# Optimization experiments

Hardware: AMD Instinct MI355X
Metric: run time of the kernel (lower is better)

The kernel has to match this reference:

```python
import jax, jax.numpy as jnp
import numpy as np

N_LAYERS = 6
EPS = 1e-5


def _s4d_layer(u, log_dt, C_re, C_im, log_A_real, A_imag, D, out_w, out_b):
    # u: (B, H, L). Standard S4D: diagonal SSM kernel -> FFT conv -> D skip -> GELU -> 1x1 conv + GLU.
    B, H, L = u.shape
    dt = jnp.exp(log_dt)                                   # (H,)
    A = -jnp.exp(log_A_real) + 1j * A_imag                 # (H, N2) complex
    dtA = A * dt[:, None]                                  # (H, N2)
    C = (C_re + 1j * C_im) * (jnp.exp(dtA) - 1.0) / A      # (H, N2) ZOH-discretized C
    V = jnp.exp(dtA[:, :, None] * jnp.arange(L))           # (H, N2, L) Vandermonde exp(dtA * l)
    k = 2.0 * jnp.einsum('hn,hnl->hl', C, V).real          # (H, L) SSM convolution kernel
    # circular conv via length-2L FFT (equivalent to causal linear conv, then truncate)
    k_f = jnp.fft.rfft(k, n=2 * L)                         # (H, L+1)
    u_f = jnp.fft.rfft(u, n=2 * L)                         # (B, H, L+1)
    y = jnp.fft.irfft(u_f * k_f, n=2 * L)[..., :L]         # (B, H, L)
    y = y + u * D[:, None]                                 # skip connection
    y = jax.nn.gelu(y, approximate=False)                  # torch nn.GELU (exact erf)
    y = jnp.einsum('bhl,gh->bgl', y, out_w) + out_b[:, None]  # 1x1 Conv1d -> (B, 2H, L)
    a, b = jnp.split(y, 2, axis=1)                         # GLU over channel dim (dim=-2)
    return a * jax.nn.sigmoid(b)


def _batchnorm(x, gamma, beta):
    # BatchNorm1d over (B, H, L): per-channel stats across batch and length (training-mode forward)
    mean = x.mean(axis=(0, 2), keepdims=True)
    var = x.var(axis=(0, 2), keepdims=True)
    return (x - mean) * jax.lax.rsqrt(var + EPS) * gamma[None, :, None] + beta[None, :, None]


def setup_inputs() -> dict:
    B, L, D_IN, H, N2 = 8, 5000, 12, 256, 32
    key = jax.random.key(0)
    ks = jax.random.split(key, 8)
    x = jax.random.normal(ks[0], (B, L, D_IN), jnp.float32)
    pre_w = jax.random.normal(ks[1], (H, D_IN), jnp.float32) / np.float32(np.sqrt(D_IN))
    pre_b = jnp.zeros((H,), jnp.float32)
    # log_dt ~ Uniform(log 0.001, log 0.1) as in S4DKernel init
    log_dt = (jax.random.uniform(ks[2], (N_LAYERS, H), jnp.float32)
              * np.float32(np.log(0.1) - np.log(0.001)) + np.float32(np.log(0.001)))
    C_re = jax.random.normal(ks[3], (N_LAYERS, H, N2), jnp.float32)
    C_im = jax.random.normal(ks[4], (N_LAYERS, H, N2), jnp.float32)
    log_A_real = jnp.full((N_LAYERS, H, N2), np.float32(np.log(0.5)), jnp.float32)
    A_imag = jnp.broadcast_to(np.float32(np.pi) * jnp.arange(N2, dtype=jnp.float32),
                              (N_LAYERS, H, N2)) + jnp.zeros((N_LAYERS, H, N2), jnp.float32)
    D = jax.random.normal(ks[5], (N_LAYERS, H), jnp.float32)
    out_w = jax.random.normal(ks[6], (N_LAYERS, 2 * H, H), jnp.float32) / np.float32(np.sqrt(H))
    out_b = jnp.zeros((N_LAYERS, 2 * H), jnp.float32)
    bn_gamma = jnp.ones((3, H), jnp.float32)
    bn_beta = jnp.zeros((3, H), jnp.float32)
    return {"x": x, "pre_w": pre_w, "pre_b": pre_b, "log_dt": log_dt, "C_re": C_re,
            "C_im": C_im, "log_A_real": log_A_real, "A_imag": A_imag, "D": D,
            "out_w": out_w, "out_b": out_b, "bn_gamma": bn_gamma, "bn_beta": bn_beta}


def reference(x, pre_w, pre_b, log_dt, C_re, C_im, log_A_real, A_imag, D, out_w, out_b, bn_gamma, bn_beta):
    h = x @ pre_w.T + pre_b          # (B, L, H) pre-projection
    h = jnp.swapaxes(h, -1, -2)      # (B, H, L)
    bn_idx = 0
    for i in range(N_LAYERS):
        z = _s4d_layer(h, log_dt[i], C_re[i], C_im[i], log_A_real[i], A_imag[i],
                       D[i], out_w[i], out_b[i])
        h = z + h                     # residual (dropout is identity in eval/reference)
        if i % 2 == 0:                # BatchNorm1d on even layers only
            h = _batchnorm(h, bn_gamma[bn_idx], bn_beta[bn_idx])
            bn_idx += 1
    return jnp.swapaxes(h, -1, -2)   # (B, L, H)
```

## Files before the change

### kernel.cpp

```cpp
#include <hip/hip_runtime.h>
#include <hip/hip_bf16.h>
#include <math.h>

#define NB 8
#define LSEQ 5000
#define DIN 12
#define HCH 256
#define N2C 32
#define NLAY 6
#define G2C 512
#define TTC 64
#define NCH 79
#define LPAD 5120

typedef __attribute__((ext_vector_type(8))) short bf8v;
typedef __attribute__((ext_vector_type(8))) unsigned short us8v;
typedef __attribute__((ext_vector_type(4))) float f32x4;

#define MFMA16(a,b,c) __builtin_amdgcn_mfma_f32_16x16x32_bf16((a),(b),(c),0,0,0)

static __device__ __forceinline__ unsigned short f2bf(float f){
  unsigned int u = __float_as_uint(f);
  u = u + 0x7FFFu + ((u >> 16) & 1u);
  return (unsigned short)(u >> 16);
}
static __device__ __forceinline__ float bf2f(unsigned short s){
  return __uint_as_float(((unsigned int)s) << 16);
}
static __device__ __forceinline__ bf8v pack8(float4 a, float4 b){
  bf8v r;
  r[0]=(short)f2bf(a.x); r[1]=(short)f2bf(a.y); r[2]=(short)f2bf(a.z); r[3]=(short)f2bf(a.w);
  r[4]=(short)f2bf(b.x); r[5]=(short)f2bf(b.y); r[6]=(short)f2bf(b.z); r[7]=(short)f2bf(b.w);
  return r;
}
static __device__ __forceinline__ float gelu_f(float x){
  return 0.5f*x*(1.0f + erff(x*0.70710678118654752f));
}
static __device__ __forceinline__ float sigm(float x){
  return 1.0f/(1.0f + expf(-x));
}


__global__ __launch_bounds__(256) void kp_params(
    const float* __restrict__ log_dt, const float* __restrict__ lAr,
    const float* __restrict__ A_im, const float* __restrict__ C_re,
    const float* __restrict__ C_im,
    float* __restrict__ p_ar, float* __restrict__ p_ai,
    float* __restrict__ p_cer, float* __restrict__ p_cei,
    float* __restrict__ p_wtr, float* __restrict__ p_wti)
{
  int idx = blockIdx.x*256 + threadIdx.x;
  int lh = idx >> 5;
  float dt = expf(log_dt[lh]);
  float Are = -expf(lAr[idx]);
  float Aim = A_im[idx];
  float ar = Are*dt, ai = Aim*dt;
  float er = expf(ar);
  float wr = er*cosf(ai), wi = er*sinf(ai);
  float inv = 1.0f/(Are*Are + Aim*Aim);
  float tr = ((wr-1.0f)*Are + wi*Aim)*inv;
  float ti = (wi*Are - (wr-1.0f)*Aim)*inv;
  p_cer[idx] = C_re[idx]*tr - C_im[idx]*ti;
  p_cei[idx] = C_re[idx]*ti + C_im[idx]*tr;
  p_ar[idx] = ar; p_ai[idx] = ai;
  float eT = expf(ar*64.0f);
  p_wtr[idx] = eT*cosf(ai*64.0f);
  p_wti[idx] = eT*sinf(ai*64.0f);
}

__global__ __launch_bounds__(256) void kp_kk(
    const float* __restrict__ p_ar, const float* __restrict__ p_ai,
    const float* __restrict__ p_cer, const float* __restrict__ p_cei,
    float* __restrict__ kk)
{
  int idx = blockIdx.x*256 + threadIdx.x;
  int d = idx & 63, lh = idx >> 6;
  int base = lh*N2C;
  float fd = (float)d;
  float s = 0.0f;
  for (int n=0; n<N2C; n++){
    float ar = p_ar[base+n], ai = p_ai[base+n];
    float e = expf(ar*fd);
    float pr = e*cosf(ai*fd), pi = e*sinf(ai*fd);
    s += p_cer[base+n]*pr - p_cei[base+n]*pi;
  }
  kk[idx] = 2.0f*s;
}

__global__ __launch_bounds__(256) void kp_A2(
    const float* __restrict__ p_ar, const float* __restrict__ p_ai,
    const float* __restrict__ p_cer, const float* __restrict__ p_cei,
    const float* __restrict__ kk, unsigned short* __restrict__ A2b)
{
  int idx = blockIdx.x*256 + threadIdx.x;
  int kcol = idx & 127;
  int t = (idx >> 7) & 63;
  int lh = idx >> 13;
  float v;
  if (kcol < 64){
    v = (kcol <= t) ? kk[lh*64 + (t - kcol)] : 0.0f;
  } else {
    int q = kcol - 64, n = q >> 1;
    int p = lh*N2C + n;
    float fp = (float)(t+1);
    float e = expf(p_ar[p]*fp);
    float pr = e*cosf(p_ai[p]*fp), pi = e*sinf(p_ai[p]*fp);
    float cer = p_cer[p], cei = p_cei[p];
    v = (q&1) ? -2.0f*(cer*pi + cei*pr) : 2.0f*(cer*pr - cei*pi);
  }
  A2b[idx] = f2bf(v);
}

__global__ __launch_bounds__(256) void kp_Vm(
    const float* __restrict__ p_ar, const float* __restrict__ p_ai,
    unsigned short* __restrict__ Vmb)
{
  int idx = blockIdx.x*256 + threadIdx.x;
  int j = idx & 63;
  int q = (idx >> 6) & 63;
  int lh = idx >> 12;
  int n = q >> 1;
  int p = lh*N2C + n;
  float fp = (float)(63 - j);
  float e = expf(p_ar[p]*fp);
  float pr = e*cosf(p_ai[p]*fp), pi = e*sinf(p_ai[p]*fp);
  Vmb[idx] = f2bf((q&1) ? pi : pr);
}

__global__ __launch_bounds__(256) void kp_Wp(
    const float* __restrict__ out_w, const float* __restrict__ out_b,
    unsigned short* __restrict__ Wpb, float* __restrict__ bp)
{
  int idx = blockIdx.x*256 + threadIdx.x;
  int hcol = idx & 255;
  int g2 = (idx >> 8) & 511;
  int li = idx >> 17;
  int src = (g2 >> 1) + ((g2 & 1) ? HCH : 0);
  Wpb[idx] = f2bf(out_w[((size_t)li*G2C + src)*HCH + hcol]);
  if (hcol == 0) bp[li*G2C + g2] = out_b[li*G2C + src];
}


__global__ __launch_bounds__(256) void k_preproj(
    const float* __restrict__ x, const float* __restrict__ pre_w,
    const float* __restrict__ pre_b, float* __restrict__ hbuf)
{
  int l = blockIdx.x*256 + threadIdx.x;
  int hc = blockIdx.y, b = blockIdx.z;
  if (l >= LSEQ) return;
  const float* xr = x + (size_t)(b*LSEQ + l)*DIN;
  const float* wr = pre_w + hc*DIN;
  float acc = pre_b[hc];
  #pragma unroll
  for (int d=0; d<DIN; d++) acc += xr[d]*wr[d];
  hbuf[(size_t)(b*HCH + hc)*LSEQ + l] = acc;
}


template<int DO_BN>
__global__ __launch_bounds__(320, 4) void k_row(
    const unsigned short* __restrict__ Vm, const unsigned short* __restrict__ A2,
    const float* __restrict__ wtr, const float* __restrict__ wti,
    const float* __restrict__ Dg, float* __restrict__ hbuf,
    const float* __restrict__ scale, const float* __restrict__ shift,
    unsigned short* __restrict__ yg, int layer)
{
  __shared__ float su[5120];
  __shared__ float sE[5120];
  int bh = blockIdx.x;
  int hc = bh & (HCH-1);
  int tid = threadIdx.x, wid = tid>>6, lane = tid&63;
  float* hrow = hbuf + (size_t)bh*LSEQ;
  float bsc = 1.0f, bsh = 0.0f;
  if (DO_BN){ bsc = scale[hc]; bsh = shift[hc]; }
  #pragma unroll
  for (int i=0;i<4;i++){
    int q = tid + i*320;
    float4 v = {0,0,0,0};
    if (q < 1250) v = *(const float4*)(hrow + q*4);
    if (DO_BN){
      v.x=v.x*bsc+bsh; v.y=v.y*bsc+bsh; v.z=v.z*bsc+bsh; v.w=v.w*bsc+bsh;
      if (q < 1250) *(float4*)(hrow + q*4) = v;
    }
    int p = q ^ (((q>>4)&7)<<1);
    *(float4*)(su + p*4) = v;
  }
  __syncthreads();

  int craw = wid*16 + (lane&15);
  int c = craw < NCH ? craw : NCH-1;
  int krow8 = (lane>>4)*8;
  int swz = (c&7)<<1;

  {
    const unsigned short* Vp = Vm + (size_t)(layer*HCH + hc)*TTC*TTC + (size_t)(lane&15)*TTC;
    f32x4 a0={0,0,0,0},a1={0,0,0,0},a2={0,0,0,0},a3={0,0,0,0};
    #pragma unroll
    for (int ks=0; ks<2; ks++){
      int kb = ks*32 + krow8;
      int p0 = (c*16 + (kb>>2)) ^ swz;
      float4 u0 = *(const float4*)(su + p0*4);
      float4 u1 = *(const float4*)(su + p0*4 + 4);
      bf8v bfr = pack8(u0,u1);
      a0 = MFMA16(*(const bf8v*)(Vp + 0*16*TTC + kb), bfr, a0);
      a1 = MFMA16(*(const bf8v*)(Vp + 1*16*TTC + kb), bfr, a1);
      a2 = MFMA16(*(const bf8v*)(Vp + 2*16*TTC + kb), bfr, a2);
      a3 = MFMA16(*(const bf8v*)(Vp + 3*16*TTC + kb), bfr, a3);
    }
    if (craw < NCH){
      int j0 = craw*16 + (lane>>4);
      int sw2 = (craw&7)<<1;
      *(f32x4*)(sE + (size_t)((j0+ 0)^sw2)*4) = a0;
      *(f32x4*)(sE + (size_t)((j0+ 4)^sw2)*4) = a1;
      *(f32x4*)(sE + (size_t)((j0+ 8)^sw2)*4) = a2;
      *(f32x4*)(sE + (size_t)((j0+12)^sw2)*4) = a3;
    }
  }
  __syncthreads();

  if (tid < 256){
    int n = tid >> 3, g = tid & 7;
    float wr = wtr[(layer*HCH+hc)*N2C + n];
    float wi = wti[(layer*HCH+hc)*N2C + n];
    int c0 = g*10;
    int cnt = NCH - c0; if (cnt > 10) cnt = 10;
    float er[10], ei[10];
    #pragma unroll
    for (int k=0;k<10;k++){
      if (k < cnt){
        int cc = c0 + k;
        int p = ((cc*16 + (n>>1)) ^ ((cc&7)<<1))*4 + (n&1)*2;
        er[k] = sE[p]; ei[k] = sE[p+1];
      } else { er[k]=0.0f; ei[k]=0.0f; }
    }
    float tr_=0.0f, ti_=0.0f;
    #pragma unroll
    for (int k=0;k<10;k++){
      if (k < cnt){
        float nr = wr*tr_ - wi*ti_ + er[k];
        ti_ = wr*ti_ + wi*tr_ + ei[k];
        tr_ = nr;
      }
    }
    float a2r = wr*wr - wi*wi,      a2i = 2.0f*wr*wi;
    float a4r = a2r*a2r - a2i*a2i,  a4i = 2.0f*a2r*a2i;
    float a8r = a4r*a4r - a4i*a4i,  a8i = 2.0f*a4r*a4i;
    float Ar = a8r*a2r - a8i*a2i,   Ai = a8r*a2i + a8i*a2r;
    float Br = tr_, Bi = ti_;
    #pragma unroll
    for (int st=1; st<8; st<<=1){
      float Ar2 = __shfl_up(Ar, st), Ai2 = __shfl_up(Ai, st);
      float Br2 = __shfl_up(Br, st), Bi2 = __shfl_up(Bi, st);
      if (g >= st){
        float nAr = Ar*Ar2 - Ai*Ai2;
        float nAi = Ar*Ai2 + Ai*Ar2;
        float nBr = Ar*Br2 - Ai*Bi2 + Br;
        float nBi = Ar*Bi2 + Ai*Br2 + Bi;
        Ar=nAr; Ai=nAi; Br=nBr; Bi=nBi;
      }
    }
    float Pr = __shfl_up(Br, 1), Pi = __shfl_up(Bi, 1);
    if (g == 0){ Pr = 0.0f; Pi = 0.0f; }
    #pragma unroll
    for (int k=0;k<10;k++){
      if (k < cnt){
        int cc = c0 + k;
        int p = ((cc*16 + (n>>1)) ^ ((cc&7)<<1))*4 + (n&1)*2;
        sE[p] = Pr; sE[p+1] = Pi;
        float nr = wr*Pr - wi*Pi + er[k];
        Pi = wr*Pi + wi*Pr + ei[k];
        Pr = nr;
      }
    }
  }
  __syncthreads();

  f32x4 acc0={0,0,0,0},acc1={0,0,0,0},acc2={0,0,0,0},acc3={0,0,0,0};
  {
    const unsigned short* Ap = A2 + (size_t)(layer*HCH + hc)*TTC*128 + (size_t)(lane&15)*128;
    #pragma unroll
    for (int ks=0; ks<2; ks++){
      int kb = ks*32 + krow8;
      int p0 = (c*16 + (kb>>2)) ^ swz;
      float4 u0 = *(const float4*)(su + p0*4);
      float4 u1 = *(const float4*)(su + p0*4 + 4);
      bf8v bfr = pack8(u0,u1);
      acc0 = MFMA16(*(const bf8v*)(Ap + 0*16*128 + kb), bfr, acc0);
      acc1 = MFMA16(*(const bf8v*)(Ap + 1*16*128 + kb), bfr, acc1);
      acc2 = MFMA16(*(const bf8v*)(Ap + 2*16*128 + kb), bfr, acc2);
      acc3 = MFMA16(*(const bf8v*)(Ap + 3*16*128 + kb), bfr, acc3);
    }
    #pragma unroll
    for (int ks=2; ks<4; ks++){
      int kb = ks*32 + krow8;
      int p0 = (c*16 + ((kb-64)>>2)) ^ swz;
      float4 s0 = *(const float4*)(sE + p0*4);
      float4 s1 = *(const float4*)(sE + p0*4 + 4);
      bf8v bhv = pack8(s0,s1);
      acc0 = MFMA16(*(const bf8v*)(Ap + 0*16*128 + kb), bhv, acc0);
      acc1 = MFMA16(*(const bf8v*)(Ap + 1*16*128 + kb), bhv, acc1);
      acc2 = MFMA16(*(const bf8v*)(Ap + 2*16*128 + kb), bhv, acc2);
      acc3 = MFMA16(*(const bf8v*)(Ap + 3*16*128 + kb), bhv, acc3);
      float4 r0, r1;
      r0.x = s0.x - bf2f(f2bf(s0.x)); r0.y = s0.y - bf2f(f2bf(s0.y));
      r0.z = s0.z - bf2f(f2bf(s0.z)); r0.w = s0.w - bf2f(f2bf(s0.w));
      r1.x = s1.x - bf2f(f2bf(s1.x)); r1.y = s1.y - bf2f(f2bf(s1.y));
      r1.z = s1.z - bf2f(f2bf(s1.z)); r1.w = s1.w - bf2f(f2bf(s1.w));
      bf8v blv = pack8(r0,r1);
      acc0 = MFMA16(*(const bf8v*)(Ap + 0*16*128 + kb), blv, acc0);
      acc1 = MFMA16(*(const bf8v*)(Ap + 1*16*128 + kb), blv, acc1);
      acc2 = MFMA16(*(const bf8v*)(Ap + 2*16*128 + kb), blv, acc2);
      acc3 = MFMA16(*(const bf8v*)(Ap + 3*16*128 + kb), blv, acc3);
    }
  }
  __syncthreads();

  {
    float* ybuf = sE;
    float Dv = Dg[layer*HCH + hc];
    int tq = (lane>>4)*4;
    int qb = craw*16 + (tq>>2);
    int sw2 = (craw&7)<<1;
    float* yb = ybuf + craw*64 + tq;
    float4 u4;
    u4 = *(const float4*)(su + (size_t)((qb+ 0)^sw2)*4);
    yb[ 0] = gelu_f(acc0[0] + Dv*u4.x); yb[ 1] = gelu_f(acc0[1] + Dv*u4.y);
    yb[ 2] = gelu_f(acc0[2] + Dv*u4.z); yb[ 3] = gelu_f(acc0[3] + Dv*u4.w);
    u4 = *(const float4*)(su + (size_t)((qb+ 4)^sw2)*4);
    yb[16] = gelu_f(acc1[0] + Dv*u4.x); yb[17] = gelu_f(acc1[1] + Dv*u4.y);
    yb[18] = gelu_f(acc1[2] + Dv*u4.z); yb[19] = gelu_f(acc1[3] + Dv*u4.w);
    u4 = *(const float4*)(su + (size_t)((qb+ 8)^sw2)*4);
    yb[32] = gelu_f(acc2[0] + Dv*u4.x); yb[33] = gelu_f(acc2[1] + Dv*u4.y);
    yb[34] = gelu_f(acc2[2] + Dv*u4.z); yb[35] = gelu_f(acc2[3] + Dv*u4.w);
    u4 = *(const float4*)(su + (size_t)((qb+12)^sw2)*4);
    yb[48] = gelu_f(acc3[0] + Dv*u4.x); yb[49] = gelu_f(acc3[1] + Dv*u4.y);
    yb[50] = gelu_f(acc3[2] + Dv*u4.z); yb[51] = gelu_f(acc3[3] + Dv*u4.w);
  }
  __syncthreads();
  unsigned short* ygp = yg + (size_t)bh*LSEQ;
  #pragma unroll
  for (int pass=0; pass<2; pass++){
    int l0 = (pass*320 + tid)*8;
    if (l0 < LSEQ){
      float4 v0 = *(const float4*)(sE + l0);
      float4 v1 = *(const float4*)(sE + l0 + 4);
      us8v o;
      o[0]=f2bf(v0.x); o[1]=f2bf(v0.y); o[2]=f2bf(v0.z); o[3]=f2bf(v0.w);
      o[4]=f2bf(v1.x); o[5]=f2bf(v1.y); o[6]=f2bf(v1.z); o[7]=f2bf(v1.w);
      *(us8v*)(ygp + l0) = o;
    }
  }
}


__global__ __launch_bounds__(256) void k_T(
    const unsigned short* __restrict__ yg, unsigned short* __restrict__ ygT)
{
  __shared__ unsigned short tile[64][72];
  int b = blockIdx.z, h0 = blockIdx.y*64, l0 = blockIdx.x*64;
  int tid = threadIdx.x;
  #pragma unroll
  for (int i=0;i<2;i++){
    int lidx = tid + i*256;
    int row = lidx>>3, c8 = (lidx&7)*8;
    us8v v = 0;
    if (l0 + c8 < LSEQ)
      v = *(const us8v*)(yg + (size_t)(b*HCH + h0 + row)*LSEQ + l0 + c8);
    *(us8v*)(&tile[row][c8]) = v;
  }
  __syncthreads();
  #pragma unroll
  for (int i=0;i<2;i++){
    int widx = tid + i*256;
    int r = widx>>3, h8 = (widx&7)*8;
    int l = l0 + r;
    us8v o = 0;
    if (l < LSEQ){
      #pragma unroll
      for (int e=0;e<8;e++) o[e] = tile[h8+e][r];
    }
    *(us8v*)(ygT + ((size_t)b*LPAD + l)*HCH + h0 + h8) = o;
  }
}


static __device__ __forceinline__ void stageA(
    const unsigned short* __restrict__ g, unsigned short* sbuf, int tid)
{
  #pragma unroll
  for (int i=0;i<8;i++){
    int p = i*256 + tid;
    int row = p>>5, kc = p&31;
    int kcl = kc ^ (row&7);
    const unsigned short* ga = g + (size_t)row*HCH + kcl*8;
    __builtin_amdgcn_global_load_lds(
        (const __attribute__((address_space(1))) void*)ga,
        (__attribute__((address_space(3))) void*)(sbuf + p*8),
        16, 0, 0);
  }
}
static __device__ __forceinline__ void stageB(
    const unsigned short* __restrict__ g, unsigned short* sbuf, int tid)
{
  #pragma unroll
  for (int i=0;i<4;i++){
    int p = i*256 + tid;
    int row = p>>5, kc = p&31;
    int kcl = kc ^ (row&7);
    const unsigned short* ga = g + (size_t)row*HCH + kcl*8;
    __builtin_amdgcn_global_load_lds(
        (const __attribute__((address_space(1))) void*)ga,
        (__attribute__((address_space(3))) void*)(sbuf + p*8),
        16, 0, 0);
  }
}
static __device__ __forceinline__ bf8v ldsF(const unsigned short* sbuf, int row, int k0){
  int byte = (row<<9) + (k0<<1);
  byte ^= ((row&7)<<4);
  return *(const bf8v*)((const char*)sbuf + byte);
}

template<int DO_STATS>
__global__ __launch_bounds__(256, 2) void k_gemm(
    const unsigned short* __restrict__ Wp, const float* __restrict__ bp,
    const unsigned short* __restrict__ ygT, float* __restrict__ hbuf,
    float* __restrict__ bnsum, float* __restrict__ bnsq, int layer)
{
  __shared__ unsigned short As[64*256];
  __shared__ unsigned short Bs[3][32*256];
  int id = blockIdx.x;
  int x = id & 7, s = id >> 3;
  int gt = s & 7;
  int q = x*8 + (s>>3);
  int b = q >> 3, lg = q & 7;
  int l0 = lg*640;

  int tid = threadIdx.x, wid = tid>>6, lane = tid&63;
  int wm = wid>>1, wn = wid&1;
  int colA = lane&15, krow8 = (lane>>4)*8;

  const unsigned short* Wt = Wp + (size_t)layer*G2C*HCH + (size_t)(gt*64)*HCH;
  const unsigned short* Yb = ygT + (size_t)b*LPAD*HCH;

  stageA(Wt, As, tid);
  stageB(Yb + (size_t)l0*HCH,      Bs[0], tid);
  stageB(Yb + (size_t)(l0+32)*HCH, Bs[1], tid);

  float4 bias4[2]; int hc0[2];
  #pragma unroll
  for (int m=0;m<2;m++){
    int g2r4 = gt*64 + wm*32 + m*16 + (lane>>4)*4;
    bias4[m] = *(const float4*)(bp + layer*G2C + g2r4);
    hc0[m] = g2r4 >> 1;
  }
  float sacc[4], qacc[4];
  if (DO_STATS){
    #pragma unroll
    for (int i=0;i<4;i++){ sacc[i]=0.0f; qacc[i]=0.0f; }
  }

  const int NT = 20;
  for (int t=0; t<NT; t++){
    __builtin_amdgcn_s_barrier();
    if (t+2 < NT)
      stageB(Yb + (size_t)(l0 + (t+2)*32)*HCH, Bs[(t+2)%3], tid);
    if (t+2 < NT)      asm volatile("s_waitcnt vmcnt(8)" ::: "memory");
    else if (t+1 < NT) asm volatile("s_waitcnt vmcnt(4)" ::: "memory");
    else               asm volatile("s_waitcnt vmcnt(0)" ::: "memory");
    __builtin_amdgcn_s_barrier();
    const unsigned short* Bc = Bs[t%3];
    f32x4 acc0 = (f32x4){0,0,0,0}, acc1 = (f32x4){0,0,0,0};
    #pragma unroll
    for (int ks=0; ks<8; ks++){
      int k0 = ks*32 + krow8;
      bf8v fb  = ldsF(Bc, wn*16 + colA, k0);
      bf8v fa0 = ldsF(As, wm*32 + colA, k0);
      bf8v fa1 = ldsF(As, wm*32 + 16 + colA, k0);
      acc0 = MFMA16(fa0, fb, acc0);
      acc1 = MFMA16(fa1, fb, acc1);
    }
    int l = l0 + t*32 + wn*16 + colA;
    #pragma unroll
    for (int m=0;m<2;m++){
      f32x4 av = m ? acc1 : acc0;
      float a0 = av[0] + bias4[m].x;
      float g0 = av[1] + bias4[m].y;
      float a1 = av[2] + bias4[m].z;
      float g1 = av[3] + bias4[m].w;
      float z0 = a0 * sigm(g0);
      float z1 = a1 * sigm(g1);
      float r0 = 0.0f, r1 = 0.0f;
      if (l < LSEQ){
        float* pp0 = hbuf + ((size_t)(b*HCH + hc0[m]))*LSEQ + l;
        float* pp1 = pp0 + LSEQ;
        r0 = z0 + pp0[0]; pp0[0] = r0;
        r1 = z1 + pp1[0]; pp1[0] = r1;
      }
      if (DO_STATS){
        sacc[m*2+0] += r0; qacc[m*2+0] += r0*r0;
        sacc[m*2+1] += r1; qacc[m*2+1] += r1*r1;
      }
    }
  }

  if (DO_STATS){
    #pragma unroll
    for (int m=0;m<2;m++){
      #pragma unroll
      for (int zr=0; zr<2; zr++){
        float sv = sacc[m*2+zr], qv = qacc[m*2+zr];
        sv += __shfl_xor(sv,1); qv += __shfl_xor(qv,1);
        sv += __shfl_xor(sv,2); qv += __shfl_xor(qv,2);
        sv += __shfl_xor(sv,4); qv += __shfl_xor(qv,4);
        sv += __shfl_xor(sv,8); qv += __shfl_xor(qv,8);
        if ((lane&15)==0){
          atomicAdd(&bnsum[hc0[m]+zr], sv);
          atomicAdd(&bnsq[hc0[m]+zr], qv);
        }
      }
    }
  }
}


__global__ void k_bnfin(const float* __restrict__ bnsum, const float* __restrict__ bnsq,
    const float* __restrict__ gam, const float* __restrict__ bet,
    float* __restrict__ scale, float* __restrict__ shift, int bnidx)
{
  int hc = threadIdx.x;
  const float inv = 1.0f/40000.0f;
  float mean = bnsum[hc]*inv;
  float var = bnsq[hc]*inv - mean*mean;
  float sc = gam[bnidx*HCH + hc] * rsqrtf(var + 1e-5f);
  scale[hc] = sc;
  shift[hc] = bet[bnidx*HCH + hc] - mean*sc;
}


__global__ __launch_bounds__(256) void k_outT(const float* __restrict__ hbuf,
    float* __restrict__ out)
{
  __shared__ float tile[64][65];
  int b = blockIdx.z, h0 = blockIdx.y*64, l0 = blockIdx.x*64;
  int tid = threadIdx.x;
  #pragma unroll
  for (int i=0;i<4;i++){
    int lidx = tid + i*256;
    int row = lidx>>4, c4 = (lidx&15)*4;
    float4 v = {0,0,0,0};
    if (l0 + c4 < LSEQ)
      v = *(const float4*)(hbuf + (size_t)(b*HCH + h0 + row)*LSEQ + l0 + c4);
    tile[row][c4+0]=v.x; tile[row][c4+1]=v.y; tile[row][c4+2]=v.z; tile[row][c4+3]=v.w;
  }
  __syncthreads();
  #pragma unroll
  for (int i=0;i<4;i++){
    int widx = tid + i*256;
    int r = widx>>4, h4 = (widx&15)*4;
    int l = l0 + r;
    if (l < LSEQ){
      float4 o = { tile[h4+0][r], tile[h4+1][r], tile[h4+2][r], tile[h4+3][r] };
      *(float4*)(out + ((size_t)(b*LSEQ) + l)*HCH + h0 + h4) = o;
    }
  }
}


extern "C" void kernel_launch(void* const* d_in, const int* in_sizes, int n_in,
                              void* d_out, int out_size, void* d_ws, size_t ws_size,
                              hipStream_t stream)
{
  (void)in_sizes; (void)n_in; (void)out_size; (void)ws_size;
  const float* x      = (const float*)d_in[0];
  const float* pre_w  = (const float*)d_in[1];
  const float* pre_b  = (const float*)d_in[2];
  const float* log_dt = (const float*)d_in[3];
  const float* C_re   = (const float*)d_in[4];
  const float* C_im   = (const float*)d_in[5];
  const float* lAr    = (const float*)d_in[6];
  const float* A_im   = (const float*)d_in[7];
  const float* Dg     = (const float*)d_in[8];
  const float* out_w  = (const float*)d_in[9];
  const float* out_b  = (const float*)d_in[10];
  const float* gam    = (const float*)d_in[11];
  const float* bet    = (const float*)d_in[12];
  float* out = (float*)d_out;

  char* ws = (char*)d_ws;
  size_t off = 0;
  auto alloc = [&](size_t bytes)->char*{
    char* p = ws + off;
    off += (bytes + 255) & ~(size_t)255;
    return p;
  };
  float*          hbuf  = (float*)         alloc((size_t)(NB*HCH*LSEQ + 8192)*4);
  unsigned short* yg    = (unsigned short*)alloc((size_t)(NB*HCH*LSEQ + 64)*2);
  unsigned short* ygT   = (unsigned short*)alloc((size_t)NB*LPAD*HCH*2);
  float*          p_ar  = (float*)         alloc((size_t)NLAY*HCH*N2C*4);
  float*          p_ai  = (float*)         alloc((size_t)NLAY*HCH*N2C*4);
  float*          p_cer = (float*)         alloc((size_t)NLAY*HCH*N2C*4);
  float*          p_cei = (float*)         alloc((size_t)NLAY*HCH*N2C*4);
  float*          p_wtr = (float*)         alloc((size_t)NLAY*HCH*N2C*4);
  float*          p_wti = (float*)         alloc((size_t)NLAY*HCH*N2C*4);
  float*          kk    = (float*)         alloc((size_t)NLAY*HCH*TTC*4);
  unsigned short* A2b   = (unsigned short*)alloc((size_t)NLAY*HCH*TTC*128*2);
  unsigned short* Vmb   = (unsigned short*)alloc((size_t)NLAY*HCH*TTC*TTC*2);
  unsigned short* Wpb   = (unsigned short*)alloc((size_t)NLAY*G2C*HCH*2);
  float*          bp    = (float*)         alloc((size_t)NLAY*G2C*4);
  float*          bnst  = (float*)         alloc((size_t)4*HCH*4);
  float* bnsum = bnst, *bnsq = bnst + HCH, *bnscale = bnst + 2*HCH, *bnshift = bnst + 3*HCH;

  kp_params<<<(NLAY*HCH*N2C)/256, 256, 0, stream>>>(log_dt, lAr, A_im, C_re, C_im,
      p_ar, p_ai, p_cer, p_cei, p_wtr, p_wti);
  kp_kk<<<(NLAY*HCH*TTC)/256, 256, 0, stream>>>(p_ar, p_ai, p_cer, p_cei, kk);
  kp_A2<<<(NLAY*HCH*TTC*128)/256, 256, 0, stream>>>(p_ar, p_ai, p_cer, p_cei, kk, A2b);
  kp_Vm<<<(NLAY*HCH*TTC*TTC)/256, 256, 0, stream>>>(p_ar, p_ai, Vmb);
  kp_Wp<<<(NLAY*G2C*HCH)/256, 256, 0, stream>>>(out_w, out_b, Wpb, bp);

  k_preproj<<<dim3(20, HCH, NB), 256, 0, stream>>>(x, pre_w, pre_b, hbuf);

  for (int layer=0; layer<NLAY; layer++){
    if (layer & 1)
      k_row<1><<<NB*HCH, 320, 0, stream>>>(Vmb, A2b, p_wtr, p_wti, Dg, hbuf,
                                           bnscale, bnshift, yg, layer);
    else
      k_row<0><<<NB*HCH, 320, 0, stream>>>(Vmb, A2b, p_wtr, p_wti, Dg, hbuf,
                                           bnscale, bnshift, yg, layer);
    k_T<<<dim3(LPAD/64, HCH/64, NB), 256, 0, stream>>>(yg, ygT);
    if ((layer & 1) == 0){
      hipMemsetAsync(bnsum, 0, 2*HCH*sizeof(float), stream);
      k_gemm<1><<<512, 256, 0, stream>>>(Wpb, bp, ygT, hbuf, bnsum, bnsq, layer);
      k_bnfin<<<1, HCH, 0, stream>>>(bnsum, bnsq, gam, bet, bnscale, bnshift, layer/2);
    } else {
      k_gemm<0><<<512, 256, 0, stream>>>(Wpb, bp, ygT, hbuf, bnsum, bnsq, layer);
    }
  }
  k_outT<<<dim3(79, HCH/64, NB), 256, 0, stream>>>(hbuf, out);
}
```

Baseline: 809.3 us.

## Remap k_row blocks per XCD and swizzle LDS accesses in k_row

Result: slower. 850.5 us (+5.1%).

```diff
diff --git a/kernel.cpp b/kernel.cpp
--- a/kernel.cpp
+++ b/kernel.cpp
@@ -167,8 +167,11 @@
 {
   __shared__ float su[5120];
   __shared__ float sE[5120];
-  int bh = blockIdx.x;
-  int hc = bh & (HCH-1);
+  int id = blockIdx.x;
+  int xcd = id & 7, local = id >> 3;
+  int hc = xcd*32 + (local >> 3);
+  int b  = local & 7;
+  int bh = b*HCH + hc;
   int tid = threadIdx.x, wid = tid>>6, lane = tid&63;
   float* hrow = hbuf + (size_t)bh*LSEQ;
   float bsc = 1.0f, bsh = 0.0f;
@@ -207,14 +210,16 @@
       a2 = MFMA16(*(const bf8v*)(Vp + 2*16*TTC + kb), bfr, a2);
       a3 = MFMA16(*(const bf8v*)(Vp + 3*16*TTC + kb), bfr, a3);
     }
-    if (craw < NCH){
-      int j0 = craw*16 + (lane>>4);
-      int sw2 = (craw&7)<<1;
-      *(f32x4*)(sE + (size_t)((j0+ 0)^sw2)*4) = a0;
-      *(f32x4*)(sE + (size_t)((j0+ 4)^sw2)*4) = a1;
-      *(f32x4*)(sE + (size_t)((j0+ 8)^sw2)*4) = a2;
-      *(f32x4*)(sE + (size_t)((j0+12)^sw2)*4) = a3;
-    }
+    if (craw >= NCH){
+      a0=(f32x4){0,0,0,0}; a1=(f32x4){0,0,0,0};
+      a2=(f32x4){0,0,0,0}; a3=(f32x4){0,0,0,0};
+    }
+    int j0 = craw*16 + (lane>>4);
+    int sw2 = (craw&7)<<1;
+    *(f32x4*)(sE + (size_t)((j0+ 0)^sw2)*4) = a0;
+    *(f32x4*)(sE + (size_t)((j0+ 4)^sw2)*4) = a1;
+    *(f32x4*)(sE + (size_t)((j0+ 8)^sw2)*4) = a2;
+    *(f32x4*)(sE + (size_t)((j0+12)^sw2)*4) = a3;
   }
   __syncthreads();
 
@@ -223,24 +228,15 @@
     float wr = wtr[(layer*HCH+hc)*N2C + n];
     float wi = wti[(layer*HCH+hc)*N2C + n];
     int c0 = g*10;
-    int cnt = NCH - c0; if (cnt > 10) cnt = 10;
-    float er[10], ei[10];
+    float tr_=0.0f, ti_=0.0f;
     #pragma unroll
     for (int k=0;k<10;k++){
-      if (k < cnt){
-        int cc = c0 + k;
-        int p = ((cc*16 + (n>>1)) ^ ((cc&7)<<1))*4 + (n&1)*2;
-        er[k] = sE[p]; ei[k] = sE[p+1];
-      } else { er[k]=0.0f; ei[k]=0.0f; }
-    }
-    float tr_=0.0f, ti_=0.0f;
-    #pragma unroll
-    for (int k=0;k<10;k++){
-      if (k < cnt){
-        float nr = wr*tr_ - wi*ti_ + er[k];
-        ti_ = wr*ti_ + wi*tr_ + ei[k];
-        tr_ = nr;
-      }
+      int cc = c0 + k;
+      int p = ((cc*16 + (n>>1)) ^ ((cc&7)<<1))*4 + (n&1)*2;
+      float2 e = *(float2*)(sE + p);
+      float nr = wr*tr_ - wi*ti_ + e.x;
+      ti_ = wr*ti_ + wi*tr_ + e.y;
+      tr_ = nr;
     }
     float a2r = wr*wr - wi*wi,      a2i = 2.0f*wr*wi;
     float a4r = a2r*a2r - a2i*a2i,  a4i = 2.0f*a2r*a2i;
@@ -263,14 +259,13 @@
     if (g == 0){ Pr = 0.0f; Pi = 0.0f; }
     #pragma unroll
     for (int k=0;k<10;k++){
-      if (k < cnt){
-        int cc = c0 + k;
-        int p = ((cc*16 + (n>>1)) ^ ((cc&7)<<1))*4 + (n&1)*2;
-        sE[p] = Pr; sE[p+1] = Pi;
-        float nr = wr*Pr - wi*Pi + er[k];
-        Pi = wr*Pi + wi*Pr + ei[k];
-        Pr = nr;
-      }
+      int cc = c0 + k;
+      int p = ((cc*16 + (n>>1)) ^ ((cc&7)<<1))*4 + (n&1)*2;
+      float2 e = *(float2*)(sE + p);
+      *(float2*)(sE + p) = make_float2(Pr, Pi);
+      float nr = wr*Pr - wi*Pi + e.x;
+      Pi = wr*Pi + wi*Pr + e.y;
+      Pr = nr;
     }
   }
   __syncthreads();
@@ -321,20 +316,23 @@
     int tq = (lane>>4)*4;
     int qb = craw*16 + (tq>>2);
     int sw2 = (craw&7)<<1;
-    float* yb = ybuf + craw*64 + tq;
-    float4 u4;
+    float4 u4, o4;
     u4 = *(const float4*)(su + (size_t)((qb+ 0)^sw2)*4);
-    yb[ 0] = gelu_f(acc0[0] + Dv*u4.x); yb[ 1] = gelu_f(acc0[1] + Dv*u4.y);
-    yb[ 2] = gelu_f(acc0[2] + Dv*u4.z); yb[ 3] = gelu_f(acc0[3] + Dv*u4.w);
+    o4.x = gelu_f(acc0[0] + Dv*u4.x); o4.y = gelu_f(acc0[1] + Dv*u4.y);
+    o4.z = gelu_f(acc0[2] + Dv*u4.z); o4.w = gelu_f(acc0[3] + Dv*u4.w);
+    *(float4*)(ybuf + (size_t)((qb+ 0)^sw2)*4) = o4;
     u4 = *(const float4*)(su + (size_t)((qb+ 4)^sw2)*4);
-    yb[16] = gelu_f(acc1[0] + Dv*u4.x); yb[17] = gelu_f(acc1[1] + Dv*u4.y);
-    yb[18] = gelu_f(acc1[2] + Dv*u4.z); yb[19] = gelu_f(acc1[3] + Dv*u4.w);
+    o4.x = gelu_f(acc1[0] + Dv*u4.x); o4.y = gelu_f(acc1[1] + Dv*u4.y);
+    o4.z = gelu_f(acc1[2] + Dv*u4.z); o4.w = gelu_f(acc1[3] + Dv*u4.w);
+    *(float4*)(ybuf + (size_t)((qb+ 4)^sw2)*4) = o4;
     u4 = *(const float4*)(su + (size_t)((qb+ 8)^sw2)*4);
-    yb[32] = gelu_f(acc2[0] + Dv*u4.x); yb[33] = gelu_f(acc2[1] + Dv*u4.y);
-    yb[34] = gelu_f(acc2[2] + Dv*u4.z); yb[35] = gelu_f(acc2[3] + Dv*u4.w);
+    o4.x = gelu_f(acc2[0] + Dv*u4.x); o4.y = gelu_f(acc2[1] + Dv*u4.y);
+    o4.z = gelu_f(acc2[2] + Dv*u4.z); o4.w = gelu_f(acc2[3] + Dv*u4.w);
+    *(float4*)(ybuf + (size_t)((qb+ 8)^sw2)*4) = o4;
     u4 = *(const float4*)(su + (size_t)((qb+12)^sw2)*4);
-    yb[48] = gelu_f(acc3[0] + Dv*u4.x); yb[49] = gelu_f(acc3[1] + Dv*u4.y);
-    yb[50] = gelu_f(acc3[2] + Dv*u4.z); yb[51] = gelu_f(acc3[3] + Dv*u4.w);
+    o4.x = gelu_f(acc3[0] + Dv*u4.x); o4.y = gelu_f(acc3[1] + Dv*u4.y);
+    o4.z = gelu_f(acc3[2] + Dv*u4.z); o4.w = gelu_f(acc3[3] + Dv*u4.w);
+    *(float4*)(ybuf + (size_t)((qb+12)^sw2)*4) = o4;
   }
   __syncthreads();
   unsigned short* ygp = yg + (size_t)bh*LSEQ;
@@ -342,8 +340,12 @@
   for (int pass=0; pass<2; pass++){
     int l0 = (pass*320 + tid)*8;
     if (l0 < LSEQ){
-      float4 v0 = *(const float4*)(sE + l0);
-      float4 v1 = *(const float4*)(sE + l0 + 4);
+      int q0 = l0 >> 2;
+      int p0 = q0 ^ (((q0>>4)&7)<<1);
+      int q1 = q0 + 1;
+      int p1 = q1 ^ (((q1>>4)&7)<<1);
+      float4 v0 = *(const float4*)(sE + (size_t)p0*4);
+      float4 v1 = *(const float4*)(sE + (size_t)p1*4);
       us8v o;
       o[0]=f2bf(v0.x); o[1]=f2bf(v0.y); o[2]=f2bf(v0.z); o[3]=f2bf(v0.w);
       o[4]=f2bf(v1.x); o[5]=f2bf(v1.y); o[6]=f2bf(v1.z); o[7]=f2bf(v1.w);
```
